# Optimization experiments

Measured on AMD Instinct MI355X. Metric: run time of the kernel, lower is better.

The kernel has to match this reference:

```python
import jax, jax.numpy as jnp
import numpy as np

TAL = 0.07
LOSS_WEIGHT = 1.0


def setup_inputs() -> dict:
    key = jax.random.key(0)
    k1, k2 = jax.random.split(key)
    feature = jax.random.normal(k1, (8192, 1024), dtype=jnp.float32)
    # labels all >= 1 so the foreground mask (label > 0) selects every row,
    # matching the original's fea = feature[label > 0] with a static shape.
    label = jax.random.randint(k2, (8192,), 1, 80, dtype=jnp.int32)
    return {"feature": feature, "label": label}


def reference(feature, label):
    # foreground=True and all labels > 0 -> fea = feature, lab = label
    fea = feature
    lab = label
    n = fea.shape[0]

    norm = jnp.linalg.norm(fea, axis=1)                      # [n]
    # ex[i, j] = <fea_i, fea_j> / (tal * ||fea_i|| * ||fea_j||)
    ex = (fea @ fea.T) / (TAL * norm[:, None] * norm[None, :])  # [n, n]

    # d_all = exp(ex); column sum pos_val + neg_val == sum_i d_all[i, j].
    # -log(d_all[i, j] / colsum_j) = logsumexp_i(ex[:, j]) - ex[i, j]
    log_colsum = jax.nn.logsumexp(ex, axis=0)                # [n]

    pos = lab[:, None] == lab[None, :]                       # pos[i, j]: lab_i == lab_j
    n_pos = jnp.sum(pos, axis=0).astype(ex.dtype)            # per-anchor positive count

    per_pair = jnp.where(pos, log_colsum[None, :] - ex, jnp.zeros((), ex.dtype))
    loss_anc = jnp.sum(per_pair, axis=0) / n_pos             # [n], mean over positives
    loss = jnp.sum(loss_anc)
    return LOSS_WEIGHT * loss / n
```

## Files before the change

kernel.cpp:

```cpp
#include <hip/hip_runtime.h>

#define TAL 0.07f
constexpr int N = 8192;
constexpr int D = 1024;
constexpr int NB = 64;
constexpr int NTILES = NB * (NB + 1) / 2;
constexpr int TPX = NTILES / 8;

typedef __bf16 bf16x8 __attribute__((ext_vector_type(8)));
typedef float f32x4 __attribute__((ext_vector_type(4)));

#define AS1 __attribute__((address_space(1)))
#define AS3 __attribute__((address_space(3)))

#define WAIT_VM(n) asm volatile("s_waitcnt vmcnt(" #n ")" ::: "memory")
#define WAIT_LGKM0 asm volatile("s_waitcnt lgkmcnt(0)" ::: "memory")
#define SCHED_FENCE __builtin_amdgcn_sched_barrier(0)
#define SBAR __builtin_amdgcn_s_barrier()

static __device__ __forceinline__ ushort f2bf(float x) {
    union { float f; uint32_t u; } c; c.f = x;
    uint32_t u = c.u;
    uint32_t r = (u + 0x7FFFu + ((u >> 16) & 1u)) >> 16;
    return (ushort)r;
}

__global__ __launch_bounds__(256) void prep_kernel(const float* __restrict__ F,
                                                   const int* __restrict__ lab,
                                                   ushort* __restrict__ Fb,
                                                   float* __restrict__ ascale,
                                                   int* __restrict__ hist) {
    int row = blockIdx.x * 4 + (threadIdx.x >> 6);
    int lane = threadIdx.x & 63;
    const float4* src = (const float4*)(F + (size_t)row * D);
    ushort4* dst = (ushort4*)(Fb + (size_t)row * D);
    float local = 0.f;
    #pragma unroll
    for (int it = 0; it < 4; ++it) {
        float4 v = src[it * 64 + lane];
        ushort4 o;
        o.x = f2bf(v.x); o.y = f2bf(v.y); o.z = f2bf(v.z); o.w = f2bf(v.w);
        dst[it * 64 + lane] = o;
        local += v.x*v.x + v.y*v.y + v.z*v.z + v.w*v.w;
    }
    #pragma unroll
    for (int off = 32; off; off >>= 1) local += __shfl_xor(local, off);
    if (lane == 0) {
        ascale[row] = rsqrtf(TAL * local);
        atomicAdd(&hist[lab[row]], 1);
    }
}

#define BM 128
#define BN 128
#define BK 32
#define TILE (BM * BK)
#define NSTEP (D / BK)

__global__ __launch_bounds__(256, 3) void gemm_kernel(const ushort* __restrict__ Fb,
                                                      const float* __restrict__ ascale,
                                                      const int* __restrict__ lab,
                                                      float* __restrict__ gSumE,
                                                      float* __restrict__ gSumP) {
    __shared__ ushort sA[3][TILE];
    __shared__ ushort sB[3][TILE];
    __shared__ float rScale[BM], cScale[BN];
    __shared__ int rLab[BM], cLab[BN];

    int kblk = blockIdx.x;
    int b = (kblk & 7) * TPX + (kblk >> 3);

    int bi = (int)((sqrtf(8.f * (float)b + 1.f) - 1.f) * 0.5f);
    while ((bi + 1) * (bi + 2) / 2 <= b) ++bi;
    while (bi * (bi + 1) / 2 > b) --bi;
    int bj = b - bi * (bi + 1) / 2;
    bool offdiag = (bi != bj);

    int I0 = bi * BM, J0 = bj * BN;
    int t = threadIdx.x;
    int lane = t & 63, w = t >> 6;
    int wr = w >> 1, wc = w & 1;

    if (t < 128) { rScale[t] = ascale[I0 + t]; rLab[t] = lab[I0 + t]; }
    else { int u = t - 128; cScale[u] = ascale[J0 + u]; cLab[u] = lab[J0 + u]; }

    f32x4 acc[4][4];
    #pragma unroll
    for (int m = 0; m < 4; ++m)
        #pragma unroll
        for (int n = 0; n < 4; ++n)
            acc[m][n] = {0.f, 0.f, 0.f, 0.f};

    int r0 = (w * 2 + 0) * 16 + (lane >> 2);
    int r1 = (w * 2 + 1) * 16 + (lane >> 2);
    int ce = (((lane & 3) ^ ((lane >> 3) & 3))) * 8;
    const ushort* srcA0 = Fb + (size_t)(I0 + r0) * D + ce;
    const ushort* srcA1 = Fb + (size_t)(I0 + r1) * D + ce;
    const ushort* srcB0 = Fb + (size_t)(J0 + r0) * D + ce;
    const ushort* srcB1 = Fb + (size_t)(J0 + r1) * D + ce;
    ushort* sAf = &sA[0][0];
    ushort* sBf = &sB[0][0];
    int d0 = (w * 2 + 0) * 512;
    int d1 = (w * 2 + 1) * 512;

#define STAGE(c, koff) do {                                                                              \
    __builtin_amdgcn_global_load_lds((const AS1 void*)(srcA0 + (koff)), (AS3 void*)(sAf + (c)*TILE + d0), 16, 0, 0); \
    __builtin_amdgcn_global_load_lds((const AS1 void*)(srcA1 + (koff)), (AS3 void*)(sAf + (c)*TILE + d1), 16, 0, 0); \
    __builtin_amdgcn_global_load_lds((const AS1 void*)(srcB0 + (koff)), (AS3 void*)(sBf + (c)*TILE + d0), 16, 0, 0); \
    __builtin_amdgcn_global_load_lds((const AS1 void*)(srcB1 + (koff)), (AS3 void*)(sBf + (c)*TILE + d1), 16, 0, 0); \
} while (0)

    int fr = lane & 15;
    int cs = ((lane >> 4) ^ ((lane >> 1) & 3)) * 8;

#define COMPUTE(cb, SECOND_BAR) do {                                                   \
    const ushort* a_ = sAf + (cb) * TILE;                                              \
    const ushort* b_ = sBf + (cb) * TILE;                                              \
    bf16x8 af[4], bfr[4];                                                              \
    _Pragma("unroll")                                                                  \
    for (int m = 0; m < 4; ++m)                                                        \
        af[m] = *(const bf16x8*)(a_ + (wr * 64 + m * 16 + fr) * BK + cs);              \
    _Pragma("unroll")                                                                  \
    for (int n = 0; n < 4; ++n)                                                        \
        bfr[n] = *(const bf16x8*)(b_ + (wc * 64 + n * 16 + fr) * BK + cs);             \
    WAIT_LGKM0; SCHED_FENCE;                                                           \
    if (SECOND_BAR) { SBAR; SCHED_FENCE; }                                             \
    _Pragma("unroll")                                                                  \
    for (int m = 0; m < 4; ++m)                                                        \
        _Pragma("unroll")                                                              \
        for (int n = 0; n < 4; ++n)                                                    \
            acc[m][n] = __builtin_amdgcn_mfma_f32_16x16x32_bf16(af[m], bfr[n], acc[m][n], 0, 0, 0); \
} while (0)

#define ITER(cb, sb, tt) do {                                                          \
    STAGE(sb, ((tt) + 2) * BK);                                                        \
    WAIT_VM(8); SCHED_FENCE; SBAR; SCHED_FENCE;                                        \
    COMPUTE(cb, 1);                                                                    \
} while (0)

    STAGE(0, 0 * BK);
    STAGE(1, 1 * BK);
    __syncthreads();

    for (int s = 0; s < NSTEP - 2; s += 3) {
        ITER(0, 2, s);
        ITER(1, 0, s + 1);
        ITER(2, 1, s + 2);
    }
    WAIT_VM(4); SCHED_FENCE; SBAR; SCHED_FENCE;
    COMPUTE(0, 0);
    WAIT_VM(0); SCHED_FENCE; SBAR; SCHED_FENCE;
    COMPUTE(1, 0);

    float rs[16]; int rl[16];
    int rbase = wr * 64 + (lane >> 4) * 4;
    #pragma unroll
    for (int m = 0; m < 4; ++m)
        #pragma unroll
        for (int r = 0; r < 4; ++r) {
            rs[m * 4 + r] = rScale[rbase + m * 16 + r];
            rl[m * 4 + r] = rLab[rbase + m * 16 + r];
        }

    const float CSH = 1.0f / TAL;
    float colE[4], colP[4], rowE[16], rowP[16];
    #pragma unroll
    for (int n = 0; n < 4; ++n) { colE[n] = 0.f; colP[n] = 0.f; }
    #pragma unroll
    for (int q = 0; q < 16; ++q) { rowE[q] = 0.f; rowP[q] = 0.f; }

    #pragma unroll
    for (int n = 0; n < 4; ++n) {
        int jl = wc * 64 + n * 16 + fr;
        float aj = cScale[jl];
        int lj = cLab[jl];
        #pragma unroll
        for (int m = 0; m < 4; ++m)
            #pragma unroll
            for (int r = 0; r < 4; ++r) {
                float ex = acc[m][n][r] * rs[m * 4 + r] * aj;
                float e = __expf(ex - CSH);
                float p = (rl[m * 4 + r] == lj) ? ex : 0.f;
                colE[n] += e; colP[n] += p;
                rowE[m * 4 + r] += e; rowP[m * 4 + r] += p;
            }
    }

    #pragma unroll
    for (int n = 0; n < 4; ++n) {
        float se = colE[n], sp = colP[n];
        se += __shfl_xor(se, 16); se += __shfl_xor(se, 32);
        sp += __shfl_xor(sp, 16); sp += __shfl_xor(sp, 32);
        if (lane < 16) {
            int jl = wc * 64 + n * 16 + lane;
            atomicAdd(&gSumE[J0 + jl], se);
            atomicAdd(&gSumP[J0 + jl], sp);
        }
    }

    if (offdiag) {
        #pragma unroll
        for (int q = 0; q < 16; ++q) {
            float se = rowE[q], sp = rowP[q];
            se += __shfl_xor(se, 1); se += __shfl_xor(se, 2);
            se += __shfl_xor(se, 4); se += __shfl_xor(se, 8);
            sp += __shfl_xor(sp, 1); sp += __shfl_xor(sp, 2);
            sp += __shfl_xor(sp, 4); sp += __shfl_xor(sp, 8);
            if ((lane & 15) == 0) {
                int row = rbase + (q >> 2) * 16 + (q & 3);
                atomicAdd(&gSumE[I0 + row], se);
                atomicAdd(&gSumP[I0 + row], sp);
            }
        }
    }
}

__global__ __launch_bounds__(256) void finalize_kernel(const float* __restrict__ gSumE,
                                                       const float* __restrict__ gSumP,
                                                       const int* __restrict__ lab,
                                                       const int* __restrict__ hist,
                                                       float* __restrict__ out) {
    int t = threadIdx.x;
    const float CSH = 1.0f / TAL;
    float local = 0.f;
    for (int j = t; j < N; j += 256) {
        float np = (float)hist[lab[j]];
        local += CSH + logf(gSumE[j]) - gSumP[j] / np;
    }
    #pragma unroll
    for (int off = 32; off; off >>= 1) local += __shfl_xor(local, off);
    __shared__ float red[4];
    if ((t & 63) == 0) red[t >> 6] = local;
    __syncthreads();
    if (t == 0) out[0] = (red[0] + red[1] + red[2] + red[3]) / (float)N;
}

extern "C" void kernel_launch(void* const* d_in, const int* in_sizes, int n_in,
                              void* d_out, int out_size, void* d_ws, size_t ws_size,
                              hipStream_t stream) {
    const float* F = (const float*)d_in[0];
    const int* lab = (const int*)d_in[1];
    float* out = (float*)d_out;
    char* ws = (char*)d_ws;

    const size_t FB_BYTES = (size_t)N * D * 2;
    ushort* Fb    = (ushort*)ws;
    float* ascale = (float*)(ws + FB_BYTES);
    float* gSumE  = (float*)(ws + FB_BYTES + 32768);
    float* gSumP  = (float*)(ws + FB_BYTES + 65536);
    int*   hist   = (int*)  (ws + FB_BYTES + 98304);

    hipMemsetAsync(ws + FB_BYTES + 32768, 0, 65536 + 512, stream);

    prep_kernel<<<N / 4, 256, 0, stream>>>(F, lab, Fb, ascale, hist);
    gemm_kernel<<<NTILES, 256, 0, stream>>>(Fb, ascale, lab, gSumE, gSumP);
    finalize_kernel<<<1, 256, 0, stream>>>(gSumE, gSumP, lab, hist, out);
}
```

Measured before the change: 246.4 us.

## Double-buffer LDS fragment reads to overlap with MFMA; parallelize finalize

The GEMM main loop now uses two register fragment sets. The LDS reads for the next k-step are issued before the MFMAs of the current step, so the ds_read latency overlaps with matrix math and the separate post-read barrier is gone. The global-load wait is tightened to vmcnt(4) and the loop is unrolled by six to rotate the buffers. The finalize kernel now runs across 32 blocks and combines results with an atomicAdd into a zeroed output, which adds a memset and makes the float summation order nondeterministic.

```diff
diff --git a/kernel.cpp b/kernel.cpp
--- a/kernel.cpp
+++ b/kernel.cpp
@@ -113,44 +113,52 @@
     int fr = lane & 15;
     int cs = ((lane >> 4) ^ ((lane >> 1) & 3)) * 8;
 
-#define COMPUTE(cb, SECOND_BAR) do {                                                   \
+#define DSREAD(AF, BF, cb) do {                                                        \
     const ushort* a_ = sAf + (cb) * TILE;                                              \
     const ushort* b_ = sBf + (cb) * TILE;                                              \
-    bf16x8 af[4], bfr[4];                                                              \
     _Pragma("unroll")                                                                  \
     for (int m = 0; m < 4; ++m)                                                        \
-        af[m] = *(const bf16x8*)(a_ + (wr * 64 + m * 16 + fr) * BK + cs);              \
+        AF[m] = *(const bf16x8*)(a_ + (wr * 64 + m * 16 + fr) * BK + cs);              \
     _Pragma("unroll")                                                                  \
     for (int n = 0; n < 4; ++n)                                                        \
-        bfr[n] = *(const bf16x8*)(b_ + (wc * 64 + n * 16 + fr) * BK + cs);             \
-    WAIT_LGKM0; SCHED_FENCE;                                                           \
-    if (SECOND_BAR) { SBAR; SCHED_FENCE; }                                             \
+        BF[n] = *(const bf16x8*)(b_ + (wc * 64 + n * 16 + fr) * BK + cs);              \
+} while (0)
+
+#define MFMA16(AF, BF) do {                                                            \
     _Pragma("unroll")                                                                  \
     for (int m = 0; m < 4; ++m)                                                        \
         _Pragma("unroll")                                                              \
         for (int n = 0; n < 4; ++n)                                                    \
-            acc[m][n] = __builtin_amdgcn_mfma_f32_16x16x32_bf16(af[m], bfr[n], acc[m][n], 0, 0, 0); \
-} while (0)
-
-#define ITER(cb, sb, tt) do {                                                          \
+            acc[m][n] = __builtin_amdgcn_mfma_f32_16x16x32_bf16(AF[m], BF[n], acc[m][n], 0, 0, 0); \
+} while (0)
+
+#define PITER(rb, sb, CA, CB, NA, NB_, tt) do {                                        \
     STAGE(sb, ((tt) + 2) * BK);                                                        \
-    WAIT_VM(8); SCHED_FENCE; SBAR; SCHED_FENCE;                                        \
-    COMPUTE(cb, 1);                                                                    \
+    WAIT_VM(4); SCHED_FENCE; SBAR; SCHED_FENCE;                                        \
+    DSREAD(NA, NB_, rb);                                                               \
+    MFMA16(CA, CB);                                                                    \
+    WAIT_LGKM0; SCHED_FENCE;                                                           \
 } while (0)
 
     STAGE(0, 0 * BK);
     STAGE(1, 1 * BK);
     __syncthreads();
-
-    for (int s = 0; s < NSTEP - 2; s += 3) {
-        ITER(0, 2, s);
-        ITER(1, 0, s + 1);
-        ITER(2, 1, s + 2);
-    }
-    WAIT_VM(4); SCHED_FENCE; SBAR; SCHED_FENCE;
-    COMPUTE(0, 0);
+    bf16x8 afA[4], bfA[4], afB[4], bfB[4];
+    DSREAD(afA, bfA, 0);
+    WAIT_LGKM0; SCHED_FENCE;
+
+    for (int s = 0; s < NSTEP - 2; s += 6) {
+        PITER(1, 2, afA, bfA, afB, bfB, s);
+        PITER(2, 0, afB, bfB, afA, bfA, s + 1);
+        PITER(0, 1, afA, bfA, afB, bfB, s + 2);
+        PITER(1, 2, afB, bfB, afA, bfA, s + 3);
+        PITER(2, 0, afA, bfA, afB, bfB, s + 4);
+        PITER(0, 1, afB, bfB, afA, bfA, s + 5);
+    }
     WAIT_VM(0); SCHED_FENCE; SBAR; SCHED_FENCE;
-    COMPUTE(1, 0);
+    DSREAD(afB, bfB, 1);
+    MFMA16(afA, bfA);
+    MFMA16(afB, bfB);
 
     float rs[16]; int rl[16];
     int rbase = wr * 64 + (lane >> 4) * 4;
@@ -221,18 +229,16 @@
                                                        const int* __restrict__ hist,
                                                        float* __restrict__ out) {
     int t = threadIdx.x;
+    int j = blockIdx.x * 256 + t;
     const float CSH = 1.0f / TAL;
-    float local = 0.f;
-    for (int j = t; j < N; j += 256) {
-        float np = (float)hist[lab[j]];
-        local += CSH + logf(gSumE[j]) - gSumP[j] / np;
-    }
+    float np = (float)hist[lab[j]];
+    float local = CSH + logf(gSumE[j]) - gSumP[j] / np;
     #pragma unroll
     for (int off = 32; off; off >>= 1) local += __shfl_xor(local, off);
     __shared__ float red[4];
     if ((t & 63) == 0) red[t >> 6] = local;
     __syncthreads();
-    if (t == 0) out[0] = (red[0] + red[1] + red[2] + red[3]) / (float)N;
+    if (t == 0) atomicAdd(out, (red[0] + red[1] + red[2] + red[3]) / (float)N);
 }
 
 extern "C" void kernel_launch(void* const* d_in, const int* in_sizes, int n_in,
@@ -251,8 +257,9 @@
     int*   hist   = (int*)  (ws + FB_BYTES + 98304);
 
     hipMemsetAsync(ws + FB_BYTES + 32768, 0, 65536 + 512, stream);
+    hipMemsetAsync(d_out, 0, sizeof(float), stream);
 
     prep_kernel<<<N / 4, 256, 0, stream>>>(F, lab, Fb, ascale, hist);
     gemm_kernel<<<NTILES, 256, 0, stream>>>(Fb, ascale, lab, gSumE, gSumP);
-    finalize_kernel<<<1, 256, 0, stream>>>(gSumE, gSumP, lab, hist, out);
-}
+    finalize_kernel<<<N / 256, 256, 0, stream>>>(gSumE, gSumP, lab, hist, out);
+}
```

New measurement: 231.3 us. -6.1%, faster.
